# Optimization experiments

Measured on AMD Instinct MI355X. Metric: run time of the kernel, lower is better.

The kernel has to match this reference:

```python
import jax, jax.numpy as jnp
import numpy as np

B, S, D, H, HD = 2, 2048, 2048, 16, 128

def _freqs_cis(dim, end, theta=10000.0):
    freqs = 1.0 / theta ** (np.arange(0, dim, 2, dtype=np.float32)[: dim // 2] / dim)
    t = np.arange(end, dtype=np.float32)
    f = np.outer(t, freqs).astype(np.float32)
    f = np.concatenate((f, f), axis=-1)
    return jnp.asarray(np.cos(f)), jnp.asarray(np.sin(f))

def _rotate_half(x):
    x1, x2 = x[..., : x.shape[-1] // 2], x[..., x.shape[-1] // 2 :]
    return jnp.concatenate((-x2, x1), axis=-1)

def setup_inputs() -> dict:
    key = jax.random.key(0)
    ks = jax.random.split(key, 5)
    x = jax.random.normal(ks[0], (B, S, D), jnp.float32)
    scale = 1.0 / np.sqrt(D)
    Wq = jax.random.normal(ks[1], (D, H, HD), jnp.float32) * scale
    Wk = jax.random.normal(ks[2], (D, H, HD), jnp.float32) * scale
    Wv = jax.random.normal(ks[3], (D, H, HD), jnp.float32) * scale
    Wo = jax.random.normal(ks[4], (H, HD, D), jnp.float32) * (1.0 / np.sqrt(D))
    mask = jnp.tril(jnp.ones((S, S), jnp.bool_))[None, None]  # causal [1,1,S,S]
    return {"x": x, "mask": mask, "Wq": Wq, "Wk": Wk, "Wv": Wv, "Wo": Wo}

def reference(x, mask, Wq, Wk, Wv, Wo):
    # QKV projections: [B,S,D] -> [B,S,H,HD]
    q = jnp.einsum('bsd,dhk->bshk', x, Wq)
    k = jnp.einsum('bsd,dhk->bshk', x, Wk)
    v = jnp.einsum('bsd,dhk->bshk', x, Wv)
    # RoPE
    cos, sin = _freqs_cis(HD, x.shape[1])
    cos = cos[None, :, None, :]
    sin = sin[None, :, None, :]
    q = q * cos + _rotate_half(q) * sin
    k = k * cos + _rotate_half(k) * sin
    # scaled dot-product attention
    scores = jnp.einsum('bqhk,bshk->bhqs', q, k) / jnp.sqrt(jnp.asarray(HD, q.dtype))
    big_neg = jnp.finfo(scores.dtype).min
    scores = jnp.where(mask, scores, big_neg)
    attn = jax.nn.softmax(scores, axis=-1)
    ctx = jnp.einsum('bhqs,bshk->bqhk', attn, v)
    # output projection contracting (heads, head_dim)
    return jnp.einsum('bqhk,hkd->bqd', ctx, Wo)
```

## Files before the change

kernel.cpp:

```cpp
#include <hip/hip_runtime.h>

typedef unsigned short u16;
typedef unsigned int u32;

constexpr int Bc = 2, Sc = 2048, Dc = 2048, Hc = 16, HDc = 128;

using short8 = __attribute__((ext_vector_type(8))) short;
using f32x4v = __attribute__((ext_vector_type(4))) float;

static __device__ __forceinline__ float bf2f(u16 v) { return __uint_as_float(((u32)v) << 16); }
static __device__ __forceinline__ u16 f2bf(float f) {
    u32 u = __float_as_uint(f);
    return (u16)((u + 0x7fffu + ((u >> 16) & 1u)) >> 16);
}

__device__ __forceinline__ void gll16(const u16* g, u16* l) {
    __builtin_amdgcn_global_load_lds((const __attribute__((address_space(1))) void*)g,
                                     (__attribute__((address_space(3))) void*)l, 16, 0, 0);
}

#define FENCE asm volatile("" ::: "memory")

__global__ __launch_bounds__(256) void rope_tab_k(float* __restrict__ ctab, float* __restrict__ stab) {
    int idx = blockIdx.x * 256 + threadIdx.x;
    int s = idx >> 6, i = idx & 63;
    float freq = exp2f(-(float)i * 0.20762050593045952f);
    float ang = (float)s * freq;
    float c, sn;
    sincosf(ang, &sn, &c);
    ctab[idx] = c;
    stab[idx] = sn;
}

__global__ __launch_bounds__(256) void cvt_k(const float* __restrict__ in, u16* __restrict__ out, int n) {
    int i = (blockIdx.x * 256 + threadIdx.x) * 8;
    if (i >= n) return;
    float4 a = *(const float4*)(in + i);
    float4 b = *(const float4*)(in + i + 4);
    u16 r[8] = {f2bf(a.x), f2bf(a.y), f2bf(a.z), f2bf(a.w),
                f2bf(b.x), f2bf(b.y), f2bf(b.z), f2bf(b.w)};
    *(uint4*)(out + i) = *(uint4*)r;
}

__global__ __launch_bounds__(256) void tcvt3_k(const float* __restrict__ in0, const float* __restrict__ in1,
                                               const float* __restrict__ in2, u16* __restrict__ out,
                                               int R, int C) {
    __shared__ u16 tile[64][68];
    const float* in = (blockIdx.z == 0) ? in0 : (blockIdx.z == 1) ? in1 : in2;
    u16* o = out + (size_t)blockIdx.z * R * C;
    int bx = blockIdx.x * 64, by = blockIdx.y * 64;
    int t = threadIdx.x;
    int r = t >> 4, c4 = (t & 15) * 4;
    #pragma unroll
    for (int i = 0; i < 4; ++i) {
        int row = by + r + i * 16;
        float4 v = *(const float4*)(in + (size_t)row * C + bx + c4);
        u16* d = &tile[r + i * 16][c4];
        d[0] = f2bf(v.x); d[1] = f2bf(v.y); d[2] = f2bf(v.z); d[3] = f2bf(v.w);
    }
    __syncthreads();
    int oc = t >> 4, r4 = (t & 15) * 4;
    #pragma unroll
    for (int i = 0; i < 4; ++i) {
        int orow = oc + i * 16;
        u16 v[4] = {tile[r4][orow], tile[r4 + 1][orow], tile[r4 + 2][orow], tile[r4 + 3][orow]};
        *(uint2*)&o[(size_t)(bx + orow) * R + by + r4] = *(const uint2*)v;
    }
}


#define QT(RB, KST, SB, VW) do { \
    short8 aF[4], bF[6]; \
    _Pragma("unroll") for (int m_ = 0; m_ < 4; ++m_) \
        aF[m_] = *(const short8*)((RB) + (wm * 64 + m_ * 16 + ln) * 32 + co); \
    _Pragma("unroll") for (int n_ = 0; n_ < 6; ++n_) \
        bF[n_] = *(const short8*)((RB) + 4096 + (wn * 96 + n_ * 16 + ln) * 32 + co); \
    if ((KST) >= 0) stage((KST), (SB)); \
    if ((VW) == 4) asm volatile("s_waitcnt vmcnt(4)" ::: "memory"); \
    else if ((VW) == 0) asm volatile("s_waitcnt vmcnt(0)" ::: "memory"); \
    FENCE; __builtin_amdgcn_s_barrier(); FENCE; \
    asm volatile("s_waitcnt lgkmcnt(0)" ::: "memory"); \
    __builtin_amdgcn_s_setprio(1); \
    _Pragma("unroll") for (int m_ = 0; m_ < 4; ++m_) \
    _Pragma("unroll") for (int n_ = 0; n_ < 6; ++n_) \
        acc[m_][n_] = __builtin_amdgcn_mfma_f32_16x16x32_bf16(aF[m_], bF[n_], acc[m_][n_], 0, 0, 0); \
    __builtin_amdgcn_s_setprio(0); \
    FENCE; __builtin_amdgcn_s_barrier(); FENCE; \
} while (0)

__global__ __launch_bounds__(512, 2) void gemm_qkv384(
        const u16* __restrict__ A, const u16* __restrict__ Bt,
        u16* __restrict__ Oq, u16* __restrict__ Ok, u16* __restrict__ Ov,
        const float* __restrict__ ctab, const float* __restrict__ stab) {
    __shared__ u16 SM[49152];
    constexpr int K = Dc;
    int t = threadIdx.x, wid = t >> 6, lane = t & 63;
    int wm = wid >> 2, wn = wid & 3;
    int ln = lane & 15, lq = lane >> 4;

    int lin = blockIdx.x;
    int swzb = (lin & 7) * 64 + (lin >> 3);
    int n0 = (swzb >> 5) * 384;
    int m0 = (swzb & 31) * 128;

    auto stage = [&](int kt, int b) {
        u16* Ad = SM + b * 16384;
        u16* Bd = SM + b * 16384 + 4096;
        {
            int row = t >> 2, cs = t & 3;
            gll16(A + (size_t)(m0 + row) * K + kt * 32 + ((cs ^ ((row >> 1) & 3)) << 3),
                  Ad + (wid * 64) * 8);
        }
        #pragma unroll
        for (int L = 0; L < 3; ++L) {
            int ci = L * 512 + t;
            int row = ci >> 2, cs = ci & 3;
            gll16(Bt + (size_t)(n0 + row) * K + kt * 32 + ((cs ^ ((row >> 1) & 3)) << 3),
                  Bd + (L * 512 + wid * 64) * 8);
        }
    };

    int co = ((lq ^ ((ln >> 1) & 3)) << 3);
    f32x4v acc[4][6] = {};

    stage(0, 0);
    stage(1, 1);
    asm volatile("s_waitcnt vmcnt(4)" ::: "memory");
    FENCE; __builtin_amdgcn_s_barrier(); FENCE;

    #pragma unroll 1
    for (int k3 = 0; k3 < 60; k3 += 3) {
        QT(SM,          k3 + 2, 2, 4);
        QT(SM + 16384,  k3 + 3, 0, 4);
        QT(SM + 32768,  k3 + 4, 1, 4);
    }
    QT(SM,          62, 2, 4);
    QT(SM + 16384,  63, 0, 4);
    QT(SM + 32768,  -1, 0, 0);
    QT(SM,          -1, 0, -1);

    int b_ = m0 >> 11;
    int s0 = m0 & (Sc - 1);
    u16* Es = SM;
    const int ESTR = 130;

    for (int c = 0; c < 3; ++c) {
        #pragma unroll
        for (int nf = 0; nf < 6; ++nf) {
            int cg = wn * 96 + nf * 16;
            if ((cg >> 7) == c) {
                int col = cg & 127;
                #pragma unroll
                for (int mf = 0; mf < 4; ++mf)
                    #pragma unroll
                    for (int r = 0; r < 4; ++r)
                        Es[(wm * 64 + mf * 16 + (lq << 2) + r) * ESTR + col + ln] =
                            f2bf(acc[mf][nf][r]);
            }
        }
        __syncthreads();

        int gcol = n0 + c * 128;
        int which = gcol >> 11;
        int h = (gcol & 2047) >> 7;
        if (which < 2) {
            u16* dst0 = which ? Ok : Oq;
            int rh = t >> 2, h2 = t & 1, jh = (t >> 1) & 1;
            int s = s0 + rh;
            const u16* rowp = Es + rh * ESTR;
            const float* ct = ctab + (size_t)s * 64;
            const float* st = stab + (size_t)s * 64;
            u16* dp = dst0 + (((size_t)(b_ * Hc + h)) * Sc + s) * HDc + h2 * 64;
            #pragma unroll
            for (int j8 = jh * 32; j8 < jh * 32 + 32; j8 += 8) {
                uint4 aa = *(const uint4*)(rowp + j8);
                uint4 bb = *(const uint4*)(rowp + 64 + j8);
                const u16* ap8 = (const u16*)&aa;
                const u16* bp8 = (const u16*)&bb;
                float4 c0f = *(const float4*)(ct + j8);
                float4 c1f = *(const float4*)(ct + j8 + 4);
                float4 sn0 = *(const float4*)(st + j8);
                float4 sn1 = *(const float4*)(st + j8 + 4);
                float cc[8] = {c0f.x, c0f.y, c0f.z, c0f.w, c1f.x, c1f.y, c1f.z, c1f.w};
                float ss[8] = {sn0.x, sn0.y, sn0.z, sn0.w, sn1.x, sn1.y, sn1.z, sn1.w};
                u16 ov[8];
                #pragma unroll
                for (int e = 0; e < 8; ++e) {
                    float x1 = bf2f(ap8[e]), x2 = bf2f(bp8[e]);
                    ov[e] = h2 ? f2bf(x2 * cc[e] + x1 * ss[e]) : f2bf(x1 * cc[e] - x2 * ss[e]);
                }
                *(uint4*)(dp + j8) = *(const uint4*)ov;
            }
        } else {
            int d = t >> 2, sh = t & 3;
            u16* dp = Ov + (((size_t)(b_ * Hc + h)) * HDc + d) * Sc + s0 + sh * 32;
            #pragma unroll
            for (int r8 = 0; r8 < 32; r8 += 8) {
                u16 ov[8];
                #pragma unroll
                for (int e = 0; e < 8; ++e)
                    ov[e] = Es[(sh * 32 + r8 + e) * ESTR + d];
                *(uint4*)(dp + r8) = *(const uint4*)ov;
            }
        }
        __syncthreads();
    }
}


#define RDA8(P) do { _Pragma("unroll") for (int m_ = 0; m_ < 4; ++m_) { \
    aF[m_][0] = *(const short8*)((P) + m_ * 1024 + co0); \
    aF[m_][1] = *(const short8*)((P) + m_ * 1024 + co1); } } while (0)

#define RDB2(P, nh) do { _Pragma("unroll") for (int j_ = 0; j_ < 2; ++j_) { \
    bF[j_][0] = *(const short8*)((P) + ((nh) * 2 + j_) * 1024 + co0); \
    bF[j_][1] = *(const short8*)((P) + ((nh) * 2 + j_) * 1024 + co1); } } while (0)

#define MFQ8(nh) do { _Pragma("unroll") for (int m_ = 0; m_ < 4; ++m_) \
    _Pragma("unroll") for (int j_ = 0; j_ < 2; ++j_) { \
    f32x4v& c_ = acc[m_][(nh) * 2 + j_]; \
    c_ = __builtin_amdgcn_mfma_f32_16x16x32_bf16(aF[m_][0], bF[j_][0], c_, 0, 0, 0); \
    c_ = __builtin_amdgcn_mfma_f32_16x16x32_bf16(aF[m_][1], bF[j_][1], c_, 0, 0, 0); } } while (0)

#define PT(nh) do { FENCE; __builtin_amdgcn_s_barrier(); FENCE; \
    asm volatile("s_waitcnt lgkmcnt(0)" ::: "memory"); \
    __builtin_amdgcn_s_setprio(1); MFQ8(nh); __builtin_amdgcn_s_setprio(0); \
    FENCE; __builtin_amdgcn_s_barrier(); FENCE; } while (0)

#define KTILE(aRb, bRb, KST, ADST, BDST, VW) do { \
    RDA8(aRb); RDB2(bRb, 0); \
    if ((KST) >= 0) stageA(KST, ADST); \
    PT(0); \
    RDB2(bRb, 1); \
    if ((KST) >= 0) stageB(KST, BDST); \
    if ((VW) == 6) asm volatile("s_waitcnt vmcnt(6)" ::: "memory"); \
    else if ((VW) == 0) asm volatile("s_waitcnt vmcnt(0)" ::: "memory"); \
    PT(1); } while (0)

__global__ __launch_bounds__(512, 2) void gemm128_op(
        const u16* __restrict__ A, const u16* __restrict__ Bt, float* __restrict__ C2) {
    __shared__ u16 SM[73728];
    constexpr int K = Dc;
    constexpr int NT = 32;
    constexpr int N = Dc;
    int t = threadIdx.x, wid = t >> 6, lane = t & 63;
    int wm = wid >> 2, wn = wid & 3;
    int ln = lane & 15, lq = lane >> 4;

    int nx = gridDim.x;
    int lin = blockIdx.y * nx + blockIdx.x;
    int cpx = (nx * gridDim.y) >> 3;
    int swzb = (lin & 7) * cpx + (lin >> 3);
    int n0 = (swzb % nx) << 8;
    int m0 = (swzb / nx) << 7;

    u16* As0 = SM;
    u16* As1 = SM + 8192;
    u16* As2 = SM + 16384;
    u16* Bs0 = SM + 24576;
    u16* Bs1 = SM + 40960;
    u16* Bs2 = SM + 57344;

    auto stageA = [&](int kt, u16* dst) {
        #pragma unroll
        for (int L = 0; L < 2; ++L) {
            int ch16 = L * 512 + wid * 64 + lane;
            int row = ch16 >> 3, ch = ch16 & 7;
            gll16(A + (size_t)(m0 + row) * K + kt * 64 + ((ch ^ (row & 7)) << 3),
                  dst + (L * 512 + wid * 64) * 8);
        }
    };
    auto stageB = [&](int kt, u16* dst) {
        #pragma unroll
        for (int L = 0; L < 4; ++L) {
            int ch16 = L * 512 + wid * 64 + lane;
            int row = ch16 >> 3, ch = ch16 & 7;
            gll16(Bt + (size_t)(n0 + row) * K + kt * 64 + ((ch ^ (row & 7)) << 3),
                  dst + (L * 512 + wid * 64) * 8);
        }
    };

    const u16* aR0 = As0 + (wm * 64 + ln) * 64;
    const u16* aR1 = As1 + (wm * 64 + ln) * 64;
    const u16* aR2 = As2 + (wm * 64 + ln) * 64;
    const u16* bR0 = Bs0 + (wn * 64 + ln) * 64;
    const u16* bR1 = Bs1 + (wn * 64 + ln) * 64;
    const u16* bR2 = Bs2 + (wn * 64 + ln) * 64;
    int sw = ln & 7;
    int co0 = (lq ^ sw) << 3;
    int co1 = ((4 | lq) ^ sw) << 3;

    short8 aF[4][2], bF[2][2];
    f32x4v acc[4][4] = {};

    stageA(0, As0); stageB(0, Bs0);
    stageA(1, As1); stageB(1, Bs1);
    asm volatile("s_waitcnt vmcnt(6)" ::: "memory");
    FENCE; __builtin_amdgcn_s_barrier(); FENCE;

    for (int k3 = 0; k3 < NT - 2; k3 += 3) {
        KTILE(aR0, bR0, k3 + 2, As2, Bs2, 6);
        KTILE(aR1, bR1, k3 + 3, As0, Bs0, 6);
        KTILE(aR2, bR2, k3 + 4, As1, Bs1, 6);
    }
    KTILE(aR0, bR0, -1, As0, Bs0, 0);
    KTILE(aR1, bR1, -1, As0, Bs0, -1);

    int rb = m0 + wm * 64 + (lq << 2);
    int cb = n0 + wn * 64 + ln;
    #pragma unroll
    for (int mf = 0; mf < 4; ++mf)
        #pragma unroll
        for (int nf = 0; nf < 4; ++nf)
            #pragma unroll
            for (int r = 0; r < 4; ++r)
                C2[(size_t)(rb + mf * 16 + r) * N + cb + nf * 16] = acc[mf][nf][r];
}

__global__ __launch_bounds__(256) void fattn_k(const u16* __restrict__ Q, const u16* __restrict__ K,
                                               const u16* __restrict__ Vt, u16* __restrict__ ctx) {
    __shared__ u16 KsA[8192];
    __shared__ u16 VsA[8192];
    __shared__ u16 PsA[4 * 32 * 72];
    int t = threadIdx.x, wid = t >> 6, lane = t & 63;
    int bh = blockIdx.x;
    int yt = blockIdx.y;
    int qi = (yt < 8) ? yt : 23 - yt;
    int q0 = qi << 7;
    int wrow0 = q0 + wid * 32;
    const u16* Qb = Q + ((size_t)bh * Sc + wrow0) * HDc;
    const u16* Kb = K + (size_t)bh * Sc * HDc;
    const u16* Vb = Vt + (size_t)bh * HDc * Sc;
    int ln = lane & 15, lq = lane >> 4;
    u16* psw = PsA + wid * 32 * 72;

    short8 aq[2][4];
    #pragma unroll
    for (int mf = 0; mf < 2; ++mf)
        #pragma unroll
        for (int ks = 0; ks < 4; ++ks)
            aq[mf][ks] = *(const short8*)(Qb + (size_t)(mf * 16 + ln) * HDc + ks * 32 + lq * 8);

    short8 onesb;
    {
        short v = (ln == 0) ? (short)0x3F80 : (short)0;
        #pragma unroll
        for (int e = 0; e < 8; ++e) onesb[e] = v;
    }

    f32x4v o[2][8] = {};
    f32x4v lacc[2] = {};

    const float sc = 0.08838834764831845f;
    const float SHIFT = 12.0f;
    int jendw = wrow0 + 31;
    int jendb = q0 + 127;
    int swz = (ln >> 1) & 3;

    for (int j0 = 0; j0 <= jendb; j0 += 64) {
        #pragma unroll
        for (int i = 0; i < 4; ++i) {
            int p = (wid * 4 + i) * 64 + lane;
            int plane = p >> 8, key = (p >> 2) & 63;
            int qc = (p & 3) ^ ((key >> 1) & 3);
            gll16(Kb + (size_t)(j0 + key) * HDc + plane * 32 + qc * 8,
                  KsA + (size_t)(wid * 4 + i) * 512);
        }
        #pragma unroll
        for (int i = 0; i < 4; ++i) {
            int p = (wid * 4 + i) * 64 + lane;
            int plane = p >> 9, d = (p >> 2) & 127;
            int qc = (p & 3) ^ ((d >> 1) & 3);
            gll16(Vb + (size_t)d * Sc + j0 + plane * 32 + qc * 8,
                  VsA + (size_t)(wid * 4 + i) * 512);
        }
        __syncthreads();

        if (j0 <= jendw) {
            f32x4v sf[2][4] = {};
            #pragma unroll
            for (int ks = 0; ks < 4; ++ks)
                #pragma unroll
                for (int nf = 0; nf < 4; ++nf) {
                    short8 bk = *(const short8*)(KsA + ks * 2048 + (nf * 16 + ln) * 32 + ((lq ^ swz) << 3));
                    sf[0][nf] = __builtin_amdgcn_mfma_f32_16x16x32_bf16(aq[0][ks], bk, sf[0][nf], 0, 0, 0);
                    sf[1][nf] = __builtin_amdgcn_mfma_f32_16x16x32_bf16(aq[1][ks], bk, sf[1][nf], 0, 0, 0);
                }

            bool diag = (j0 + 63 > wrow0);
            #pragma unroll
            for (int mf = 0; mf < 2; ++mf) {
                int rowb = mf * 16 + (lq << 2);
                #pragma unroll
                for (int nf = 0; nf < 4; ++nf) {
                    int col = nf * 16 + ln;
                    int ck = col >> 3, cl = col & 7;
                    #pragma unroll
                    for (int r = 0; r < 4; ++r) {
                        float p = __expf(fmaf(sf[mf][nf][r], sc, -SHIFT));
                        if (diag && (j0 + col > wrow0 + rowb + r)) p = 0.f;
                        int row = rowb + r;
                        psw[row * 72 + ((ck ^ (row & 7)) << 3) + cl] = f2bf(p);
                    }
                }
            }

            short8 ap0[2][2];
            #pragma unroll
            for (int mf = 0; mf < 2; ++mf)
                #pragma unroll
                for (int ks = 0; ks < 2; ++ks)
                    ap0[mf][ks] = *(const short8*)(psw + (mf * 16 + ln) * 72 + (((ks * 4 + lq) ^ (ln & 7)) << 3));
            #pragma unroll
            for (int ks = 0; ks < 2; ++ks) {
                lacc[0] = __builtin_amdgcn_mfma_f32_16x16x32_bf16(ap0[0][ks], onesb, lacc[0], 0, 0, 0);
                lacc[1] = __builtin_amdgcn_mfma_f32_16x16x32_bf16(ap0[1][ks], onesb, lacc[1], 0, 0, 0);
                #pragma unroll
                for (int nd = 0; nd < 8; ++nd) {
                    short8 bv = *(const short8*)(VsA + ks * 4096 + (nd * 16 + ln) * 32 + ((lq ^ swz) << 3));
                    o[0][nd] = __builtin_amdgcn_mfma_f32_16x16x32_bf16(ap0[0][ks], bv, o[0][nd], 0, 0, 0);
                    o[1][nd] = __builtin_amdgcn_mfma_f32_16x16x32_bf16(ap0[1][ks], bv, o[1][nd], 0, 0, 0);
                }
            }
        }
        __syncthreads();
    }

    int b = bh >> 4, h = bh & 15;
    #pragma unroll
    for (int mf = 0; mf < 2; ++mf)
        #pragma unroll
        for (int r = 0; r < 4; ++r) {
            float lv = __shfl(lacc[mf][r], lane & 48, 64);
            float inv = 1.0f / lv;
            int q = wrow0 + mf * 16 + (lq << 2) + r;
            u16* cp = ctx + (((size_t)(b * Sc + q)) * Hc + h) * HDc + ln;
            #pragma unroll
            for (int nd = 0; nd < 8; ++nd)
                cp[nd * 16] = f2bf(o[mf][nd][r] * inv);
        }
}

extern "C" void kernel_launch(void* const* d_in, const int* in_sizes, int n_in,
                              void* d_out, int out_size, void* d_ws, size_t ws_size,
                              hipStream_t stream) {
    (void)in_sizes; (void)n_in; (void)out_size; (void)ws_size;
    const float* x  = (const float*)d_in[0];
    const float* Wq = (const float*)d_in[2];
    const float* Wk = (const float*)d_in[3];
    const float* Wv = (const float*)d_in[4];
    const float* Wo = (const float*)d_in[5];

    char* w = (char*)d_ws;
    u16* Wt  = (u16*)w; w += (size_t)3 * Dc * Dc * 2;
    u16* Qb  = (u16*)w; w += (size_t)Bc * Hc * Sc * HDc * 2;
    u16* Kb  = (u16*)w; w += (size_t)Bc * Hc * Sc * HDc * 2;
    u16* Vb  = (u16*)w; w += (size_t)Bc * Hc * Sc * HDc * 2;
    u16* ctx = (u16*)w; w += (size_t)Bc * Sc * Hc * HDc * 2;
    float* ctab = (float*)w; w += (size_t)Sc * 64 * 4;
    float* stab = (float*)w; w += (size_t)Sc * 64 * 4;
    u16* xb = (u16*)d_out;

    rope_tab_k<<<dim3(Sc * 64 / 256), 256, 0, stream>>>(ctab, stab);

    int nx = Bc * Sc * Dc;
    cvt_k<<<dim3(nx / 2048), 256, 0, stream>>>(x, xb, nx);

    tcvt3_k<<<dim3(Dc / 64, Dc / 64, 3), 256, 0, stream>>>(Wq, Wk, Wv, Wt, Dc, Dc);
    gemm_qkv384<<<dim3(512), 512, 0, stream>>>(xb, Wt, Qb, Kb, Vb, ctab, stab);

    fattn_k<<<dim3(Bc * Hc, Sc / 128), 256, 0, stream>>>(Qb, Kb, Vb, ctx);

    tcvt3_k<<<dim3(Dc / 64, Dc / 64, 1), 256, 0, stream>>>(Wo, Wo, Wo, Wt, Dc, Dc);
    gemm128_op<<<dim3(Dc / 256, (Bc * Sc) / 128), 512, 0, stream>>>(
        ctx, Wt, (float*)d_out);
}
```

Measured before the change: 393.6 us.

## Deepen QKV GEMM K-step to 64 and double-buffer K/V tiles in attention

The QKV projection GEMM moves from a triple-buffered 32-wide K step to a double-buffered 64-wide K step. Each tile is split into sub-phases whose async global-to-LDS loads are interleaved with half-tile MFMA batches, which means fewer barriers per unit of K. The flash-attention kernel now double-buffers its K/V LDS tiles so the next key block's loads overlap the current block's compute, and the P scratch stride drops from 72 to 64. LDS use grows in both kernels, which may cut occupancy, and the tighter P stride may bring back bank conflicts.

After: 405.0 us. 2.9% more time.

```diff
diff --git a/kernel.cpp b/kernel.cpp
--- a/kernel.cpp
+++ b/kernel.cpp
@@ -20,6 +20,7 @@
 }
 
 #define FENCE asm volatile("" ::: "memory")
+#define BARX do { FENCE; __builtin_amdgcn_s_barrier(); FENCE; } while (0)
 
 __global__ __launch_bounds__(256) void rope_tab_k(float* __restrict__ ctab, float* __restrict__ stab) {
     int idx = blockIdx.x * 256 + threadIdx.x;
@@ -69,30 +70,42 @@
 }
 
 
-#define QT(RB, KST, SB, VW) do { \
-    short8 aF[4], bF[6]; \
-    _Pragma("unroll") for (int m_ = 0; m_ < 4; ++m_) \
-        aF[m_] = *(const short8*)((RB) + (wm * 64 + m_ * 16 + ln) * 32 + co); \
-    _Pragma("unroll") for (int n_ = 0; n_ < 6; ++n_) \
-        bF[n_] = *(const short8*)((RB) + 4096 + (wn * 96 + n_ * 16 + ln) * 32 + co); \
-    if ((KST) >= 0) stage((KST), (SB)); \
-    if ((VW) == 4) asm volatile("s_waitcnt vmcnt(4)" ::: "memory"); \
-    else if ((VW) == 0) asm volatile("s_waitcnt vmcnt(0)" ::: "memory"); \
-    FENCE; __builtin_amdgcn_s_barrier(); FENCE; \
-    asm volatile("s_waitcnt lgkmcnt(0)" ::: "memory"); \
-    __builtin_amdgcn_s_setprio(1); \
-    _Pragma("unroll") for (int m_ = 0; m_ < 4; ++m_) \
-    _Pragma("unroll") for (int n_ = 0; n_ < 6; ++n_) \
-        acc[m_][n_] = __builtin_amdgcn_mfma_f32_16x16x32_bf16(aF[m_], bF[n_], acc[m_][n_], 0, 0, 0); \
-    __builtin_amdgcn_s_setprio(0); \
-    FENCE; __builtin_amdgcn_s_barrier(); FENCE; \
+#define VRD_A(pb, ks) do { _Pragma("unroll") for (int m_ = 0; m_ < 4; ++m_) \
+    aF[m_] = *(const short8*)((pb) + (ks) * 4096 + (wm * 64 + m_ * 16 + ln) * 32 + co); } while (0)
+
+#define VRD_B(pb, nh, ks) do { _Pragma("unroll") for (int j_ = 0; j_ < 3; ++j_) \
+    bF[j_] = *(const short8*)((pb) + 8192 + (ks) * 12288 + (wn * 96 + (nh) * 48 + j_ * 16 + ln) * 32 + co); } while (0)
+
+#define VMF(nh) do { _Pragma("unroll") for (int m_ = 0; m_ < 4; ++m_) \
+    _Pragma("unroll") for (int j_ = 0; j_ < 3; ++j_) \
+        acc[m_][(nh) * 3 + j_] = __builtin_amdgcn_mfma_f32_16x16x32_bf16(aF[m_], bF[j_], acc[m_][(nh) * 3 + j_], 0, 0, 0); } while (0)
+
+#define MTAIL(nh) do { asm volatile("s_waitcnt lgkmcnt(0)" ::: "memory"); \
+    __builtin_amdgcn_s_setprio(1); VMF(nh); __builtin_amdgcn_s_setprio(0); BARX; } while (0)
+
+#define QTILE(pb, kt1, b1, TAIL) do { \
+    VRD_A(pb, 0); VRD_B(pb, 0, 0); \
+    if (!(TAIL)) { SA(kt1, b1, 0); SB(kt1, b1, 0, 0); } \
+    BARX; MTAIL(0); \
+    VRD_B(pb, 1, 0); \
+    if (!(TAIL)) { SB(kt1, b1, 0, 1); SB(kt1, b1, 0, 2); \
+        asm volatile("s_waitcnt vmcnt(4)" ::: "memory"); } \
+    else asm volatile("s_waitcnt vmcnt(0)" ::: "memory"); \
+    BARX; MTAIL(1); \
+    VRD_A(pb, 1); VRD_B(pb, 0, 1); \
+    if (!(TAIL)) { SA(kt1, b1, 1); SB(kt1, b1, 1, 0); \
+        asm volatile("s_waitcnt vmcnt(2)" ::: "memory"); } \
+    BARX; MTAIL(0); \
+    VRD_B(pb, 1, 1); \
+    if (!(TAIL)) { SB(kt1, b1, 1, 1); SB(kt1, b1, 1, 2); } \
+    BARX; MTAIL(1); \
 } while (0)
 
-__global__ __launch_bounds__(512, 2) void gemm_qkv384(
+__global__ __launch_bounds__(512, 2) void gemm_qkv64(
         const u16* __restrict__ A, const u16* __restrict__ Bt,
         u16* __restrict__ Oq, u16* __restrict__ Ok, u16* __restrict__ Ov,
         const float* __restrict__ ctab, const float* __restrict__ stab) {
-    __shared__ u16 SM[49152];
+    __shared__ u16 SM[65536];
     constexpr int K = Dc;
     int t = threadIdx.x, wid = t >> 6, lane = t & 63;
     int wm = wid >> 2, wn = wid & 3;
@@ -103,41 +116,37 @@
     int n0 = (swzb >> 5) * 384;
     int m0 = (swzb & 31) * 128;
 
-    auto stage = [&](int kt, int b) {
-        u16* Ad = SM + b * 16384;
-        u16* Bd = SM + b * 16384 + 4096;
-        {
-            int row = t >> 2, cs = t & 3;
-            gll16(A + (size_t)(m0 + row) * K + kt * 32 + ((cs ^ ((row >> 1) & 3)) << 3),
-                  Ad + (wid * 64) * 8);
-        }
-        #pragma unroll
-        for (int L = 0; L < 3; ++L) {
-            int ci = L * 512 + t;
-            int row = ci >> 2, cs = ci & 3;
-            gll16(Bt + (size_t)(n0 + row) * K + kt * 32 + ((cs ^ ((row >> 1) & 3)) << 3),
-                  Bd + (L * 512 + wid * 64) * 8);
-        }
+    auto SA = [&](int kt, int b, int ks) {
+        int p = t;
+        int row = p >> 2, cs = p & 3;
+        gll16(A + (size_t)(m0 + row) * K + kt * 64 + ks * 32 + ((cs ^ ((row >> 1) & 3)) << 3),
+              SM + b * 32768 + ks * 4096 + (wid * 64) * 8);
     };
+    auto SB = [&](int kt, int b, int ks, int L) {
+        int p = L * 512 + t;
+        int row = p >> 2, cs = p & 3;
+        gll16(Bt + (size_t)(n0 + row) * K + kt * 64 + ks * 32 + ((cs ^ ((row >> 1) & 3)) << 3),
+              SM + b * 32768 + 8192 + ks * 12288 + (L * 512 + wid * 64) * 8);
+    };
 
     int co = ((lq ^ ((ln >> 1) & 3)) << 3);
+    short8 aF[4], bF[3];
     f32x4v acc[4][6] = {};
 
-    stage(0, 0);
-    stage(1, 1);
+    SA(0, 0, 0); SB(0, 0, 0, 0); SB(0, 0, 0, 1); SB(0, 0, 0, 2);
+    SA(0, 0, 1); SB(0, 0, 1, 0); SB(0, 0, 1, 1); SB(0, 0, 1, 2);
     asm volatile("s_waitcnt vmcnt(4)" ::: "memory");
-    FENCE; __builtin_amdgcn_s_barrier(); FENCE;
+    BARX;
 
     #pragma unroll 1
-    for (int k3 = 0; k3 < 60; k3 += 3) {
-        QT(SM,          k3 + 2, 2, 4);
-        QT(SM + 16384,  k3 + 3, 0, 4);
-        QT(SM + 32768,  k3 + 4, 1, 4);
-    }
-    QT(SM,          62, 2, 4);
-    QT(SM + 16384,  63, 0, 4);
-    QT(SM + 32768,  -1, 0, 0);
-    QT(SM,          -1, 0, -1);
+    for (int kt = 0; kt < 30; kt += 2) {
+        QTILE(SM,         kt + 1, 1, 0);
+        QTILE(SM + 32768, kt + 2, 0, 0);
+    }
+    QTILE(SM,         31, 1, 0);
+    QTILE(SM + 32768,  0, 0, 1);
+
+    __syncthreads();
 
     int b_ = m0 >> 11;
     int s0 = m0 & (Sc - 1);
@@ -209,23 +218,23 @@
 
 
 #define RDA8(P) do { _Pragma("unroll") for (int m_ = 0; m_ < 4; ++m_) { \
-    aF[m_][0] = *(const short8*)((P) + m_ * 1024 + co0); \
-    aF[m_][1] = *(const short8*)((P) + m_ * 1024 + co1); } } while (0)
+    aG[m_][0] = *(const short8*)((P) + m_ * 1024 + co0); \
+    aG[m_][1] = *(const short8*)((P) + m_ * 1024 + co1); } } while (0)
 
 #define RDB2(P, nh) do { _Pragma("unroll") for (int j_ = 0; j_ < 2; ++j_) { \
-    bF[j_][0] = *(const short8*)((P) + ((nh) * 2 + j_) * 1024 + co0); \
-    bF[j_][1] = *(const short8*)((P) + ((nh) * 2 + j_) * 1024 + co1); } } while (0)
+    bG[j_][0] = *(const short8*)((P) + ((nh) * 2 + j_) * 1024 + co0); \
+    bG[j_][1] = *(const short8*)((P) + ((nh) * 2 + j_) * 1024 + co1); } } while (0)
 
 #define MFQ8(nh) do { _Pragma("unroll") for (int m_ = 0; m_ < 4; ++m_) \
     _Pragma("unroll") for (int j_ = 0; j_ < 2; ++j_) { \
     f32x4v& c_ = acc[m_][(nh) * 2 + j_]; \
-    c_ = __builtin_amdgcn_mfma_f32_16x16x32_bf16(aF[m_][0], bF[j_][0], c_, 0, 0, 0); \
-    c_ = __builtin_amdgcn_mfma_f32_16x16x32_bf16(aF[m_][1], bF[j_][1], c_, 0, 0, 0); } } while (0)
-
-#define PT(nh) do { FENCE; __builtin_amdgcn_s_barrier(); FENCE; \
+    c_ = __builtin_amdgcn_mfma_f32_16x16x32_bf16(aG[m_][0], bG[j_][0], c_, 0, 0, 0); \
+    c_ = __builtin_amdgcn_mfma_f32_16x16x32_bf16(aG[m_][1], bG[j_][1], c_, 0, 0, 0); } } while (0)
+
+#define PT(nh) do { BARX; \
     asm volatile("s_waitcnt lgkmcnt(0)" ::: "memory"); \
     __builtin_amdgcn_s_setprio(1); MFQ8(nh); __builtin_amdgcn_s_setprio(0); \
-    FENCE; __builtin_amdgcn_s_barrier(); FENCE; } while (0)
+    BARX; } while (0)
 
 #define KTILE(aRb, bRb, KST, ADST, BDST, VW) do { \
     RDA8(aRb); RDB2(bRb, 0); \
@@ -290,13 +299,13 @@
     int co0 = (lq ^ sw) << 3;
     int co1 = ((4 | lq) ^ sw) << 3;
 
-    short8 aF[4][2], bF[2][2];
+    short8 aG[4][2], bG[2][2];
     f32x4v acc[4][4] = {};
 
     stageA(0, As0); stageB(0, Bs0);
     stageA(1, As1); stageB(1, Bs1);
     asm volatile("s_waitcnt vmcnt(6)" ::: "memory");
-    FENCE; __builtin_amdgcn_s_barrier(); FENCE;
+    BARX;
 
     for (int k3 = 0; k3 < NT - 2; k3 += 3) {
         KTILE(aR0, bR0, k3 + 2, As2, Bs2, 6);
@@ -319,9 +328,9 @@
 
 __global__ __launch_bounds__(256) void fattn_k(const u16* __restrict__ Q, const u16* __restrict__ K,
                                                const u16* __restrict__ Vt, u16* __restrict__ ctx) {
-    __shared__ u16 KsA[8192];
-    __shared__ u16 VsA[8192];
-    __shared__ u16 PsA[4 * 32 * 72];
+    __shared__ u16 KsA[2 * 8192];
+    __shared__ u16 VsA[2 * 8192];
+    __shared__ u16 PsA[4 * 32 * 64];
     int t = threadIdx.x, wid = t >> 6, lane = t & 63;
     int bh = blockIdx.x;
     int yt = blockIdx.y;
@@ -332,7 +341,7 @@
     const u16* Kb = K + (size_t)bh * Sc * HDc;
     const u16* Vb = Vt + (size_t)bh * HDc * Sc;
     int ln = lane & 15, lq = lane >> 4;
-    u16* psw = PsA + wid * 32 * 72;
+    u16* psw = PsA + wid * 2048;
 
     short8 aq[2][4];
     #pragma unroll
@@ -357,32 +366,47 @@
     int jendb = q0 + 127;
     int swz = (ln >> 1) & 3;
 
-    for (int j0 = 0; j0 <= jendb; j0 += 64) {
+    auto stageKV = [&](int j0s, int buf) {
+        u16* Kd = KsA + buf * 8192;
+        u16* Vd = VsA + buf * 8192;
         #pragma unroll
         for (int i = 0; i < 4; ++i) {
             int p = (wid * 4 + i) * 64 + lane;
             int plane = p >> 8, key = (p >> 2) & 63;
             int qc = (p & 3) ^ ((key >> 1) & 3);
-            gll16(Kb + (size_t)(j0 + key) * HDc + plane * 32 + qc * 8,
-                  KsA + (size_t)(wid * 4 + i) * 512);
+            gll16(Kb + (size_t)(j0s + key) * HDc + plane * 32 + qc * 8,
+                  Kd + (size_t)(wid * 4 + i) * 512);
         }
         #pragma unroll
         for (int i = 0; i < 4; ++i) {
             int p = (wid * 4 + i) * 64 + lane;
             int plane = p >> 9, d = (p >> 2) & 127;
             int qc = (p & 3) ^ ((d >> 1) & 3);
-            gll16(Vb + (size_t)d * Sc + j0 + plane * 32 + qc * 8,
-                  VsA + (size_t)(wid * 4 + i) * 512);
-        }
-        __syncthreads();
+            gll16(Vb + (size_t)d * Sc + j0s + plane * 32 + qc * 8,
+                  Vd + (size_t)(wid * 4 + i) * 512);
+        }
+    };
+
+    stageKV(0, 0);
+    for (int j0 = 0; j0 <= jendb; j0 += 64) {
+        int cur = (j0 >> 6) & 1;
+        if (j0 + 64 <= jendb) {
+            stageKV(j0 + 64, cur ^ 1);
+            asm volatile("s_waitcnt vmcnt(8)" ::: "memory");
+        } else {
+            asm volatile("s_waitcnt vmcnt(0)" ::: "memory");
+        }
+        BARX;
 
         if (j0 <= jendw) {
+            const u16* Kc = KsA + cur * 8192;
+            const u16* Vc = VsA + cur * 8192;
             f32x4v sf[2][4] = {};
             #pragma unroll
             for (int ks = 0; ks < 4; ++ks)
                 #pragma unroll
                 for (int nf = 0; nf < 4; ++nf) {
-                    short8 bk = *(const short8*)(KsA + ks * 2048 + (nf * 16 + ln) * 32 + ((lq ^ swz) << 3));
+                    short8 bk = *(const short8*)(Kc + ks * 2048 + (nf * 16 + ln) * 32 + ((lq ^ swz) << 3));
                     sf[0][nf] = __builtin_amdgcn_mfma_f32_16x16x32_bf16(aq[0][ks], bk, sf[0][nf], 0, 0, 0);
                     sf[1][nf] = __builtin_amdgcn_mfma_f32_16x16x32_bf16(aq[1][ks], bk, sf[1][nf], 0, 0, 0);
                 }
@@ -400,7 +424,7 @@
                         float p = __expf(fmaf(sf[mf][nf][r], sc, -SHIFT));
                         if (diag && (j0 + col > wrow0 + rowb + r)) p = 0.f;
                         int row = rowb + r;
-                        psw[row * 72 + ((ck ^ (row & 7)) << 3) + cl] = f2bf(p);
+                        psw[row * 64 + ((ck ^ (row & 7)) << 3) + cl] = f2bf(p);
                     }
                 }
             }
@@ -410,20 +434,20 @@
             for (int mf = 0; mf < 2; ++mf)
                 #pragma unroll
                 for (int ks = 0; ks < 2; ++ks)
-                    ap0[mf][ks] = *(const short8*)(psw + (mf * 16 + ln) * 72 + (((ks * 4 + lq) ^ (ln & 7)) << 3));
+                    ap0[mf][ks] = *(const short8*)(psw + (mf * 16 + ln) * 64 + (((ks * 4 + lq) ^ (ln & 7)) << 3));
             #pragma unroll
             for (int ks = 0; ks < 2; ++ks) {
                 lacc[0] = __builtin_amdgcn_mfma_f32_16x16x32_bf16(ap0[0][ks], onesb, lacc[0], 0, 0, 0);
                 lacc[1] = __builtin_amdgcn_mfma_f32_16x16x32_bf16(ap0[1][ks], onesb, lacc[1], 0, 0, 0);
                 #pragma unroll
                 for (int nd = 0; nd < 8; ++nd) {
-                    short8 bv = *(const short8*)(VsA + ks * 4096 + (nd * 16 + ln) * 32 + ((lq ^ swz) << 3));
+                    short8 bv = *(const short8*)(Vc + ks * 4096 + (nd * 16 + ln) * 32 + ((lq ^ swz) << 3));
                     o[0][nd] = __builtin_amdgcn_mfma_f32_16x16x32_bf16(ap0[0][ks], bv, o[0][nd], 0, 0, 0);
                     o[1][nd] = __builtin_amdgcn_mfma_f32_16x16x32_bf16(ap0[1][ks], bv, o[1][nd], 0, 0, 0);
                 }
             }
         }
-        __syncthreads();
+        BARX;
     }
 
     int b = bh >> 4, h = bh & 15;
@@ -467,7 +491,7 @@
     cvt_k<<<dim3(nx / 2048), 256, 0, stream>>>(x, xb, nx);
 
     tcvt3_k<<<dim3(Dc / 64, Dc / 64, 3), 256, 0, stream>>>(Wq, Wk, Wv, Wt, Dc, Dc);
-    gemm_qkv384<<<dim3(512), 512, 0, stream>>>(xb, Wt, Qb, Kb, Vb, ctab, stab);
+    gemm_qkv64<<<dim3(512), 512, 0, stream>>>(xb, Wt, Qb, Kb, Vb, ctab, stab);
 
     fattn_k<<<dim3(Bc * Hc, Sc / 128), 256, 0, stream>>>(Qb, Kb, Vb, ctx);
 
```

## Double-buffer K/V tiles in flash attention and shrink per-wave P scratch

Applied to the files above, without the earlier changes.

The attention kernel now double-buffers K and V tiles in shared memory. It prefetches the next 64-key block with async global-to-LDS loads while computing on the current one, replacing the synchronous load-then-syncthreads pattern with vmcnt waits and raw barriers. The P staging buffer is shrunk to 32 columns and processed in two halves, each followed immediately by its PV MFMAs, and exp is rewritten as exp2 with prescaled constants. The trade is double the K/V LDS footprint, which may lower occupancy. The GEMM kernels only get cosmetic macro and variable renames.

Result: slower. 419.4 us (+6.6%).

```diff
diff --git a/kernel.cpp b/kernel.cpp
--- a/kernel.cpp
+++ b/kernel.cpp
@@ -20,6 +20,7 @@
 }
 
 #define FENCE asm volatile("" ::: "memory")
+#define BARX do { FENCE; __builtin_amdgcn_s_barrier(); FENCE; } while (0)
 
 __global__ __launch_bounds__(256) void rope_tab_k(float* __restrict__ ctab, float* __restrict__ stab) {
     int idx = blockIdx.x * 256 + threadIdx.x;
@@ -78,14 +79,14 @@
     if ((KST) >= 0) stage((KST), (SB)); \
     if ((VW) == 4) asm volatile("s_waitcnt vmcnt(4)" ::: "memory"); \
     else if ((VW) == 0) asm volatile("s_waitcnt vmcnt(0)" ::: "memory"); \
-    FENCE; __builtin_amdgcn_s_barrier(); FENCE; \
+    BARX; \
     asm volatile("s_waitcnt lgkmcnt(0)" ::: "memory"); \
     __builtin_amdgcn_s_setprio(1); \
     _Pragma("unroll") for (int m_ = 0; m_ < 4; ++m_) \
     _Pragma("unroll") for (int n_ = 0; n_ < 6; ++n_) \
         acc[m_][n_] = __builtin_amdgcn_mfma_f32_16x16x32_bf16(aF[m_], bF[n_], acc[m_][n_], 0, 0, 0); \
     __builtin_amdgcn_s_setprio(0); \
-    FENCE; __builtin_amdgcn_s_barrier(); FENCE; \
+    BARX; \
 } while (0)
 
 __global__ __launch_bounds__(512, 2) void gemm_qkv384(
@@ -126,7 +127,7 @@
     stage(0, 0);
     stage(1, 1);
     asm volatile("s_waitcnt vmcnt(4)" ::: "memory");
-    FENCE; __builtin_amdgcn_s_barrier(); FENCE;
+    BARX;
 
     #pragma unroll 1
     for (int k3 = 0; k3 < 60; k3 += 3) {
@@ -209,23 +210,23 @@
 
 
 #define RDA8(P) do { _Pragma("unroll") for (int m_ = 0; m_ < 4; ++m_) { \
-    aF[m_][0] = *(const short8*)((P) + m_ * 1024 + co0); \
-    aF[m_][1] = *(const short8*)((P) + m_ * 1024 + co1); } } while (0)
+    aG[m_][0] = *(const short8*)((P) + m_ * 1024 + co0); \
+    aG[m_][1] = *(const short8*)((P) + m_ * 1024 + co1); } } while (0)
 
 #define RDB2(P, nh) do { _Pragma("unroll") for (int j_ = 0; j_ < 2; ++j_) { \
-    bF[j_][0] = *(const short8*)((P) + ((nh) * 2 + j_) * 1024 + co0); \
-    bF[j_][1] = *(const short8*)((P) + ((nh) * 2 + j_) * 1024 + co1); } } while (0)
+    bG[j_][0] = *(const short8*)((P) + ((nh) * 2 + j_) * 1024 + co0); \
+    bG[j_][1] = *(const short8*)((P) + ((nh) * 2 + j_) * 1024 + co1); } } while (0)
 
 #define MFQ8(nh) do { _Pragma("unroll") for (int m_ = 0; m_ < 4; ++m_) \
     _Pragma("unroll") for (int j_ = 0; j_ < 2; ++j_) { \
     f32x4v& c_ = acc[m_][(nh) * 2 + j_]; \
-    c_ = __builtin_amdgcn_mfma_f32_16x16x32_bf16(aF[m_][0], bF[j_][0], c_, 0, 0, 0); \
-    c_ = __builtin_amdgcn_mfma_f32_16x16x32_bf16(aF[m_][1], bF[j_][1], c_, 0, 0, 0); } } while (0)
-
-#define PT(nh) do { FENCE; __builtin_amdgcn_s_barrier(); FENCE; \
+    c_ = __builtin_amdgcn_mfma_f32_16x16x32_bf16(aG[m_][0], bG[j_][0], c_, 0, 0, 0); \
+    c_ = __builtin_amdgcn_mfma_f32_16x16x32_bf16(aG[m_][1], bG[j_][1], c_, 0, 0, 0); } } while (0)
+
+#define PT(nh) do { BARX; \
     asm volatile("s_waitcnt lgkmcnt(0)" ::: "memory"); \
     __builtin_amdgcn_s_setprio(1); MFQ8(nh); __builtin_amdgcn_s_setprio(0); \
-    FENCE; __builtin_amdgcn_s_barrier(); FENCE; } while (0)
+    BARX; } while (0)
 
 #define KTILE(aRb, bRb, KST, ADST, BDST, VW) do { \
     RDA8(aRb); RDB2(bRb, 0); \
@@ -290,13 +291,13 @@
     int co0 = (lq ^ sw) << 3;
     int co1 = ((4 | lq) ^ sw) << 3;
 
-    short8 aF[4][2], bF[2][2];
+    short8 aG[4][2], bG[2][2];
     f32x4v acc[4][4] = {};
 
     stageA(0, As0); stageB(0, Bs0);
     stageA(1, As1); stageB(1, Bs1);
     asm volatile("s_waitcnt vmcnt(6)" ::: "memory");
-    FENCE; __builtin_amdgcn_s_barrier(); FENCE;
+    BARX;
 
     for (int k3 = 0; k3 < NT - 2; k3 += 3) {
         KTILE(aR0, bR0, k3 + 2, As2, Bs2, 6);
@@ -319,9 +320,9 @@
 
 __global__ __launch_bounds__(256) void fattn_k(const u16* __restrict__ Q, const u16* __restrict__ K,
                                                const u16* __restrict__ Vt, u16* __restrict__ ctx) {
-    __shared__ u16 KsA[8192];
-    __shared__ u16 VsA[8192];
-    __shared__ u16 PsA[4 * 32 * 72];
+    __shared__ u16 KsA[2 * 8192];
+    __shared__ u16 VsA[2 * 8192];
+    __shared__ u16 PsA[4 * 32 * 32];
     int t = threadIdx.x, wid = t >> 6, lane = t & 63;
     int bh = blockIdx.x;
     int yt = blockIdx.y;
@@ -332,7 +333,7 @@
     const u16* Kb = K + (size_t)bh * Sc * HDc;
     const u16* Vb = Vt + (size_t)bh * HDc * Sc;
     int ln = lane & 15, lq = lane >> 4;
-    u16* psw = PsA + wid * 32 * 72;
+    u16* psw = PsA + wid * 1024;
 
     short8 aq[2][4];
     #pragma unroll
@@ -351,79 +352,93 @@
     f32x4v o[2][8] = {};
     f32x4v lacc[2] = {};
 
-    const float sc = 0.08838834764831845f;
-    const float SHIFT = 12.0f;
+    const float sc2 = 0.12751726861f;
+    const float SHIFT2 = 17.312340490667f;
     int jendw = wrow0 + 31;
     int jendb = q0 + 127;
     int swz = (ln >> 1) & 3;
 
-    for (int j0 = 0; j0 <= jendb; j0 += 64) {
+    auto stageKV = [&](int j0s, int buf) {
+        u16* Kd = KsA + buf * 8192;
+        u16* Vd = VsA + buf * 8192;
         #pragma unroll
         for (int i = 0; i < 4; ++i) {
             int p = (wid * 4 + i) * 64 + lane;
             int plane = p >> 8, key = (p >> 2) & 63;
             int qc = (p & 3) ^ ((key >> 1) & 3);
-            gll16(Kb + (size_t)(j0 + key) * HDc + plane * 32 + qc * 8,
-                  KsA + (size_t)(wid * 4 + i) * 512);
+            gll16(Kb + (size_t)(j0s + key) * HDc + plane * 32 + qc * 8,
+                  Kd + (size_t)(wid * 4 + i) * 512);
         }
         #pragma unroll
         for (int i = 0; i < 4; ++i) {
             int p = (wid * 4 + i) * 64 + lane;
             int plane = p >> 9, d = (p >> 2) & 127;
             int qc = (p & 3) ^ ((d >> 1) & 3);
-            gll16(Vb + (size_t)d * Sc + j0 + plane * 32 + qc * 8,
-                  VsA + (size_t)(wid * 4 + i) * 512);
-        }
-        __syncthreads();
+            gll16(Vb + (size_t)d * Sc + j0s + plane * 32 + qc * 8,
+                  Vd + (size_t)(wid * 4 + i) * 512);
+        }
+    };
+
+    stageKV(0, 0);
+    for (int j0 = 0; j0 <= jendb; j0 += 64) {
+        int cur = (j0 >> 6) & 1;
+        if (j0 + 64 <= jendb) {
+            stageKV(j0 + 64, cur ^ 1);
+            asm volatile("s_waitcnt vmcnt(8)" ::: "memory");
+        } else {
+            asm volatile("s_waitcnt vmcnt(0)" ::: "memory");
+        }
+        BARX;
 
         if (j0 <= jendw) {
+            const u16* Kc = KsA + cur * 8192;
+            const u16* Vc = VsA + cur * 8192;
             f32x4v sf[2][4] = {};
             #pragma unroll
             for (int ks = 0; ks < 4; ++ks)
                 #pragma unroll
                 for (int nf = 0; nf < 4; ++nf) {
-                    short8 bk = *(const short8*)(KsA + ks * 2048 + (nf * 16 + ln) * 32 + ((lq ^ swz) << 3));
+                    short8 bk = *(const short8*)(Kc + ks * 2048 + (nf * 16 + ln) * 32 + ((lq ^ swz) << 3));
                     sf[0][nf] = __builtin_amdgcn_mfma_f32_16x16x32_bf16(aq[0][ks], bk, sf[0][nf], 0, 0, 0);
                     sf[1][nf] = __builtin_amdgcn_mfma_f32_16x16x32_bf16(aq[1][ks], bk, sf[1][nf], 0, 0, 0);
                 }
 
             bool diag = (j0 + 63 > wrow0);
-            #pragma unroll
-            for (int mf = 0; mf < 2; ++mf) {
-                int rowb = mf * 16 + (lq << 2);
-                #pragma unroll
-                for (int nf = 0; nf < 4; ++nf) {
-                    int col = nf * 16 + ln;
-                    int ck = col >> 3, cl = col & 7;
+            short8 ap0[2];
+            #pragma unroll
+            for (int h = 0; h < 2; ++h) {
+                #pragma unroll
+                for (int nf2 = 0; nf2 < 2; ++nf2) {
+                    int nf = h * 2 + nf2;
                     #pragma unroll
-                    for (int r = 0; r < 4; ++r) {
-                        float p = __expf(fmaf(sf[mf][nf][r], sc, -SHIFT));
-                        if (diag && (j0 + col > wrow0 + rowb + r)) p = 0.f;
-                        int row = rowb + r;
-                        psw[row * 72 + ((ck ^ (row & 7)) << 3) + cl] = f2bf(p);
+                    for (int mf = 0; mf < 2; ++mf) {
+                        int rowb = mf * 16 + (lq << 2);
+                        int col = nf * 16 + ln;
+                        int c = nf2 * 16 + ln;
+                        int ck = c >> 3, cl = c & 7;
+                        #pragma unroll
+                        for (int r = 0; r < 4; ++r) {
+                            float p = exp2f(fmaf(sf[mf][nf][r], sc2, -SHIFT2));
+                            if (diag && (j0 + col > wrow0 + rowb + r)) p = 0.f;
+                            int row = rowb + r;
+                            psw[row * 32 + ((ck ^ (row & 3)) << 3) + cl] = f2bf(p);
+                        }
                     }
                 }
-            }
-
-            short8 ap0[2][2];
-            #pragma unroll
-            for (int mf = 0; mf < 2; ++mf)
-                #pragma unroll
-                for (int ks = 0; ks < 2; ++ks)
-                    ap0[mf][ks] = *(const short8*)(psw + (mf * 16 + ln) * 72 + (((ks * 4 + lq) ^ (ln & 7)) << 3));
-            #pragma unroll
-            for (int ks = 0; ks < 2; ++ks) {
-                lacc[0] = __builtin_amdgcn_mfma_f32_16x16x32_bf16(ap0[0][ks], onesb, lacc[0], 0, 0, 0);
-                lacc[1] = __builtin_amdgcn_mfma_f32_16x16x32_bf16(ap0[1][ks], onesb, lacc[1], 0, 0, 0);
+                #pragma unroll
+                for (int mf = 0; mf < 2; ++mf)
+                    ap0[mf] = *(const short8*)(psw + (mf * 16 + ln) * 32 + ((lq ^ (ln & 3)) << 3));
+                lacc[0] = __builtin_amdgcn_mfma_f32_16x16x32_bf16(ap0[0], onesb, lacc[0], 0, 0, 0);
+                lacc[1] = __builtin_amdgcn_mfma_f32_16x16x32_bf16(ap0[1], onesb, lacc[1], 0, 0, 0);
                 #pragma unroll
                 for (int nd = 0; nd < 8; ++nd) {
-                    short8 bv = *(const short8*)(VsA + ks * 4096 + (nd * 16 + ln) * 32 + ((lq ^ swz) << 3));
-                    o[0][nd] = __builtin_amdgcn_mfma_f32_16x16x32_bf16(ap0[0][ks], bv, o[0][nd], 0, 0, 0);
-                    o[1][nd] = __builtin_amdgcn_mfma_f32_16x16x32_bf16(ap0[1][ks], bv, o[1][nd], 0, 0, 0);
+                    short8 bv = *(const short8*)(Vc + h * 4096 + (nd * 16 + ln) * 32 + ((lq ^ swz) << 3));
+                    o[0][nd] = __builtin_amdgcn_mfma_f32_16x16x32_bf16(ap0[0], bv, o[0][nd], 0, 0, 0);
+                    o[1][nd] = __builtin_amdgcn_mfma_f32_16x16x32_bf16(ap0[1], bv, o[1][nd], 0, 0, 0);
                 }
             }
         }
-        __syncthreads();
+        BARX;
     }
 
     int b = bh >> 4, h = bh & 15;
```
